# Optimization experiments

Measured on AMD Instinct MI355X. Metric: run time of the kernel, lower is better.

## Reference

```python
import jax, jax.numpy as jnp
import numpy as np


def setup_inputs() -> dict:
    key = jax.random.key(0)
    k1, k2, k3 = jax.random.split(key, 3)
    B, S, E = 2, 2048, 2048
    H, O, A = 16, 1024, 128  # heads, codebook options, head_size (E = H*A)
    x = jax.random.normal(k1, (B, S, E), dtype=jnp.float32)
    vq_head_weights = jax.random.normal(k2, (H, O, A), dtype=jnp.float32) * 0.02
    vq_codebooks = jax.random.normal(k3, (H, O, A), dtype=jnp.float32) * 0.02
    temperature = jnp.ones((1,), dtype=jnp.float32)
    return {"x": x, "vq_head_weights": vq_head_weights, "vq_codebooks": vq_codebooks, "temperature": temperature}


def reference(x, vq_head_weights, vq_codebooks, temperature):
    # Training-mode, frozen, use_temperature=True path (straight-through VQ):
    # probs = one_hot(argmax(logits)) + softmax(logits/T) - stop_grad(softmax(logits/T))
    B, S, E = x.shape
    H, O, A = vq_head_weights.shape
    x_prepped = x.reshape(B, S, H, A)
    logits = jnp.einsum('bsha,hoa->bsho', x_prepped, vq_head_weights)
    probs = jax.nn.softmax(logits / temperature[0], axis=-1)
    argmax = jnp.argmax(logits, axis=-1)  # [B,S,H]
    hard_probs = jax.nn.one_hot(argmax, O, dtype=logits.dtype)
    probs = hard_probs + probs - jax.lax.stop_gradient(probs)
    out = jnp.einsum('bsho,hoa->bsha', probs, vq_codebooks)
    return out.reshape(B, S, E)
```

## Files before the change

### kernel.cpp

```cpp
#include <hip/hip_runtime.h>

typedef _Float16 half8 __attribute__((ext_vector_type(8)));
typedef float    f32x16 __attribute__((ext_vector_type(16)));

constexpr int kH = 16;
constexpr int kO = 1024;
constexpr int kA = 128;
constexpr int kBS = 4096;
constexpr int MTILE = 64;
constexpr int NITER = 16;

__global__ void split_w(const float* __restrict__ w, ushort* __restrict__ wp) {
    const int lane = threadIdx.x & 63;
    const int gw   = blockIdx.x * 4 + (threadIdx.x >> 6);
    const int ks   = lane >> 3;
    const int half = (lane >> 2) & 1;
    const int j    = (2 * lane) & 7;
#pragma unroll
    for (int q = 0; q < 4; ++q) {
        int r = gw * 4 + q;
        int h = r >> 10, o = r & 1023, t = o >> 5, o31 = o & 31;
        float2 v = *(const float2*)(w + r * kA + lane * 2);
        _Float16 h0 = (_Float16)v.x, h1 = (_Float16)v.y;
        _Float16 l0 = (_Float16)(v.x - (float)h0), l1 = (_Float16)(v.y - (float)h1);
        ushort2 hv = { __builtin_bit_cast(ushort, h0), __builtin_bit_cast(ushort, h1) };
        ushort2 lv = { __builtin_bit_cast(ushort, l0), __builtin_bit_cast(ushort, l1) };
        ushort* d = wp + (h * 32 + t) * 8192 + ks * 512 + (half * 32 + o31) * 8 + j;
        *(ushort2*)d = hv;
        *(ushort2*)(d + 4096) = lv;
    }
}

__launch_bounds__(256, 2)
__global__ void vq_argmax_gather(const float* __restrict__ x,
                                 const ushort* __restrict__ wp,
                                 const float* __restrict__ cb,
                                 float* __restrict__ out) {
    __shared__ float red_max[2][MTILE];
    __shared__ int   red_idx[2][MTILE];

    const int tid   = threadIdx.x;
    const int lane  = tid & 63;
    const int wv    = tid >> 6;
    const int nhalf = wv >> 1;
    const int mtile = wv & 1;
    const int bid   = blockIdx.x;
    const int h  = ((bid & 7) << 1) | ((bid >> 3) & 1);
    const int p0 = (bid >> 4) * MTILE;

    const int l31  = lane & 31;
    const int half = lane >> 5;

    const ushort* wbase = wp + (h * 32 + nhalf * 16) * 8192 + lane * 8;

    uint4 bufA[16], bufB[16];
    auto loadTile = [&](uint4* buf, int it) {
        const ushort* p = wbase + it * 8192;
#pragma unroll
        for (int ks = 0; ks < 8; ++ks) {
            buf[ks]     = *(const uint4*)(p + ks * 512);
            buf[8 + ks] = *(const uint4*)(p + 4096 + ks * 512);
        }
    };

    loadTile(bufA, 0);

    const int mrow = p0 + mtile * 32 + l31;
    const float* xbase = x + (mrow * kH + h) * kA + half * 8;
    half8 xh[8], xl[8];
#pragma unroll
    for (int ks = 0; ks < 8; ++ks) {
        float4 v0 = *(const float4*)(xbase + ks * 16);
        float4 v1 = *(const float4*)(xbase + ks * 16 + 4);
        float va[8] = { v0.x, v0.y, v0.z, v0.w, v1.x, v1.y, v1.z, v1.w };
        half8 hi, lo;
#pragma unroll
        for (int j = 0; j < 8; ++j) {
            _Float16 hj = (_Float16)va[j];
            hi[j] = hj;
            lo[j] = (_Float16)(va[j] - (float)hj);
        }
        xh[ks] = hi; xl[ks] = lo;
    }

    float best = -1e30f;
    int   bidx = 0;
    const int nwb = nhalf * (kO / 2);

    auto computeTile = [&](const uint4* buf, int it) {
        f32x16 acc = {};
#pragma unroll
        for (int ks = 0; ks < 8; ++ks)
            acc = __builtin_amdgcn_mfma_f32_32x32x16_f16(
                __builtin_bit_cast(half8, buf[ks]), xh[ks], acc, 0, 0, 0);
#pragma unroll
        for (int ks = 0; ks < 8; ++ks)
            acc = __builtin_amdgcn_mfma_f32_32x32x16_f16(
                __builtin_bit_cast(half8, buf[ks]), xl[ks], acc, 0, 0, 0);
#pragma unroll
        for (int ks = 0; ks < 8; ++ks)
            acc = __builtin_amdgcn_mfma_f32_32x32x16_f16(
                __builtin_bit_cast(half8, buf[8 + ks]), xh[ks], acc, 0, 0, 0);
        float lv = acc[0];
        int   lr = 0;
#pragma unroll
        for (int r = 1; r < 16; ++r) {
            if (acc[r] > lv) { lv = acc[r]; lr = r; }
        }
        int li = nwb + it * 32 + 4 * half + (lr & 3) + 8 * (lr >> 2);
        if (lv > best) { best = lv; bidx = li; }
    };

    for (int it2 = 0; it2 < NITER; it2 += 2) {
        loadTile(bufB, it2 + 1);
        computeTile(bufA, it2);
        if (it2 + 2 < NITER) loadTile(bufA, it2 + 2);
        computeTile(bufB, it2 + 1);
    }

    {
        float om = __shfl_xor(best, 32, 64);
        int   oi = __shfl_xor(bidx, 32, 64);
        if (om > best || (om == best && oi < bidx)) { best = om; bidx = oi; }
    }
    if (half == 0) {
        red_max[nhalf][mtile * 32 + l31] = best;
        red_idx[nhalf][mtile * 32 + l31] = bidx;
    }
    __syncthreads();

    for (int i = tid; i < MTILE * 32; i += 256) {
        int row = i >> 5, ch = i & 31;
        float m0 = red_max[0][row], m1 = red_max[1][row];
        int o = (m1 > m0) ? red_idx[1][row] : red_idx[0][row];
        float4 v = *(const float4*)(cb + (h * kO + o) * kA + ch * 4);
        *(float4*)(out + ((p0 + row) * kH + h) * kA + ch * 4) = v;
    }
}

extern "C" void kernel_launch(void* const* d_in, const int* in_sizes, int n_in,
                              void* d_out, int out_size, void* d_ws, size_t ws_size,
                              hipStream_t stream) {
    const float* x  = (const float*)d_in[0];
    const float* w  = (const float*)d_in[1];
    const float* cb = (const float*)d_in[2];
    float* out = (float*)d_out;

    ushort* wpacked = (ushort*)d_ws;

    split_w<<<dim3(1024), dim3(256), 0, stream>>>(w, wpacked);
    vq_argmax_gather<<<dim3((kBS / MTILE) * kH), dim3(256), 0, stream>>>(x, wpacked, cb, out);
}
```

Baseline: 159.4 us.

## Stage weight tiles through LDS with async global_load_lds double buffering

Replaces per-wave register prefetch of packed fp16 hi/lo weight tiles with asynchronous global-to-LDS copies into a double-buffered shared tile. The tile is shared by the two M-tile waves that use the same weight half, and per-iteration barriers sync the buffers. The aim is to halve redundant global weight loads and free the large uint4 register buffers. The cost is 64KB of LDS per block, which may limit occupancy, plus an added barrier each iteration.

```diff
diff --git a/kernel.cpp b/kernel.cpp
--- a/kernel.cpp
+++ b/kernel.cpp
@@ -9,6 +9,9 @@
 constexpr int kBS = 4096;
 constexpr int MTILE = 64;
 constexpr int NITER = 16;
+
+typedef const __attribute__((address_space(1))) uint32_t* gas_ptr;
+typedef __attribute__((address_space(3))) uint32_t* las_ptr;
 
 __global__ void split_w(const float* __restrict__ w, ushort* __restrict__ wp) {
     const int lane = threadIdx.x & 63;
@@ -36,6 +39,7 @@
                                  const ushort* __restrict__ wp,
                                  const float* __restrict__ cb,
                                  float* __restrict__ out) {
+    __shared__ ushort wtile[2][2][8192];
     __shared__ float red_max[2][MTILE];
     __shared__ int   red_idx[2][MTILE];
 
@@ -51,19 +55,21 @@
     const int l31  = lane & 31;
     const int half = lane >> 5;
 
-    const ushort* wbase = wp + (h * 32 + nhalf * 16) * 8192 + lane * 8;
+    const ushort* wh_base = wp + h * 32 * 8192;
 
-    uint4 bufA[16], bufB[16];
-    auto loadTile = [&](uint4* buf, int it) {
-        const ushort* p = wbase + it * 8192;
+    auto stage = [&](int it, int buf) {
 #pragma unroll
-        for (int ks = 0; ks < 8; ++ks) {
-            buf[ks]     = *(const uint4*)(p + ks * 512);
-            buf[8 + ks] = *(const uint4*)(p + 4096 + ks * 512);
+        for (int q = 0; q < 8; ++q) {
+            int c   = wv * 8 + q;
+            int nh  = c >> 4, rem = c & 15;
+            const ushort* g = wh_base + (nh * 16 + it) * 8192 + rem * 512 + lane * 8;
+            ushort* l = &wtile[buf][nh][rem * 512];
+            __builtin_amdgcn_global_load_lds((gas_ptr)(const void*)g,
+                                             (las_ptr)(void*)l, 16, 0, 0);
         }
     };
 
-    loadTile(bufA, 0);
+    stage(0, 0);
 
     const int mrow = p0 + mtile * 32 + l31;
     const float* xbase = x + (mrow * kH + h) * kA + half * 8;
@@ -87,20 +93,30 @@
     int   bidx = 0;
     const int nwb = nhalf * (kO / 2);
 
-    auto computeTile = [&](const uint4* buf, int it) {
+    __syncthreads();
+
+    for (int it = 0; it < NITER; ++it) {
+        const int cur = it & 1;
+        if (it + 1 < NITER) stage(it + 1, cur ^ 1);
+
+        const ushort* lbase = &wtile[cur][nhalf][lane * 8];
+        half8 wh[8], wl[8];
+#pragma unroll
+        for (int ks = 0; ks < 8; ++ks) {
+            wh[ks] = *(const half8*)(lbase + ks * 512);
+            wl[ks] = *(const half8*)(lbase + 4096 + ks * 512);
+        }
         f32x16 acc = {};
 #pragma unroll
         for (int ks = 0; ks < 8; ++ks)
-            acc = __builtin_amdgcn_mfma_f32_32x32x16_f16(
-                __builtin_bit_cast(half8, buf[ks]), xh[ks], acc, 0, 0, 0);
+            acc = __builtin_amdgcn_mfma_f32_32x32x16_f16(wh[ks], xh[ks], acc, 0, 0, 0);
 #pragma unroll
         for (int ks = 0; ks < 8; ++ks)
-            acc = __builtin_amdgcn_mfma_f32_32x32x16_f16(
-                __builtin_bit_cast(half8, buf[ks]), xl[ks], acc, 0, 0, 0);
+            acc = __builtin_amdgcn_mfma_f32_32x32x16_f16(wh[ks], xl[ks], acc, 0, 0, 0);
 #pragma unroll
         for (int ks = 0; ks < 8; ++ks)
-            acc = __builtin_amdgcn_mfma_f32_32x32x16_f16(
-                __builtin_bit_cast(half8, buf[8 + ks]), xh[ks], acc, 0, 0, 0);
+            acc = __builtin_amdgcn_mfma_f32_32x32x16_f16(wl[ks], xh[ks], acc, 0, 0, 0);
+
         float lv = acc[0];
         int   lr = 0;
 #pragma unroll
@@ -109,13 +125,8 @@
         }
         int li = nwb + it * 32 + 4 * half + (lr & 3) + 8 * (lr >> 2);
         if (lv > best) { best = lv; bidx = li; }
-    };
 
-    for (int it2 = 0; it2 < NITER; it2 += 2) {
-        loadTile(bufB, it2 + 1);
-        computeTile(bufA, it2);
-        if (it2 + 2 < NITER) loadTile(bufA, it2 + 2);
-        computeTile(bufB, it2 + 1);
+        __syncthreads();
     }
 
     {
```

New measurement: 153.0 us. 4.0% less time.
